# Optimization experiments

Hardware: AMD Instinct MI355X
Metric: run time of the kernel (lower is better)

The kernel has to match this reference:

```python
import jax, jax.numpy as jnp
import numpy as np

SCALE = 32.0
MARGIN = 0.25


def setup_inputs() -> dict:
    key = jax.random.key(0)
    k1, k2 = jax.random.split(key)
    feats = jax.random.normal(k1, (8192, 128), dtype=jnp.float32)
    labels = jax.random.randint(k2, (8192,), 0, 14, dtype=jnp.int64)
    return {"feats": feats, "labels": labels}


def reference(feats, labels):
    # cosine similarity: L2-normalize rows then GEMM  -> sim [B, B]
    f = feats / jnp.linalg.norm(feats, axis=1, keepdims=True)
    sim = f @ f.T

    B = feats.shape[0]
    same = labels[:, None] == labels[None, :]
    eye = jnp.eye(B, dtype=bool)
    pos_mask = same & ~eye          # same label, excluding self
    neg_mask = ~same                # different label

    s, m = SCALE, MARGIN
    alpha_p = jax.nn.relu(1.0 + m - sim)
    alpha_n = jax.nn.relu(sim + m)
    # exponents; masked-out entries set to -inf so exp -> 0 (matches masked sum)
    expo_p = jnp.where(pos_mask, -s * alpha_p * (sim - (1.0 - m)), -jnp.inf)
    expo_n = jnp.where(neg_mask, s * alpha_n * (sim - m), -jnp.inf)

    loss_p = jnp.sum(jnp.exp(expo_p), axis=1)   # [B]
    loss_n = jnp.sum(jnp.exp(expo_n), axis=1)   # [B]
    loss = jnp.mean(jnp.log1p(loss_p * loss_n))
    return loss
```

## Files before the change

kernel.cpp:

```cpp
#include <hip/hip_runtime.h>
#include <math.h>


#define DIM 128
typedef short bf16x8 __attribute__((ext_vector_type(8)));
typedef float f32x4 __attribute__((ext_vector_type(4)));

#if __has_builtin(__builtin_amdgcn_exp2f)
#define EXP2F __builtin_amdgcn_exp2f
#else
#define EXP2F exp2f
#endif

__device__ __forceinline__ unsigned short f2bf(float f) {
    unsigned int b = __float_as_uint(f);
    unsigned int r = (b + 0x7FFFu + ((b >> 16) & 1u)) >> 16;
    return (unsigned short)r;
}
__device__ __forceinline__ unsigned int packPN(float p, float n) {
    return (unsigned int)f2bf(p) | ((unsigned int)f2bf(n) << 16);
}

__global__ void prep_kernel(const float* __restrict__ feats,
                            unsigned int* __restrict__ featsN, int B) {
    int wave = (blockIdx.x * blockDim.x + threadIdx.x) >> 6;
    int lane = threadIdx.x & 63;
    if (wave >= B) return;
    const float2* rp = (const float2*)(feats + (size_t)wave * DIM);
    float2 v = rp[lane];
    float s = v.x * v.x + v.y * v.y;
#pragma unroll
    for (int off = 32; off; off >>= 1) s += __shfl_xor(s, off);
    float inv = rsqrtf(s);
    featsN[(size_t)wave * 64 + lane] =
        (unsigned int)f2bf(v.x * inv) | ((unsigned int)f2bf(v.y * inv) << 16);
}

__global__ __launch_bounds__(256, 3) void circle_main_kernel(
    const unsigned short* __restrict__ featsN, const int* __restrict__ labels,
    unsigned int* __restrict__ partial, int B) {
    __shared__ unsigned char smem[49152] __attribute__((aligned(16)));
    unsigned char* Al = smem;
    unsigned char* Bl = smem + 32768;
    unsigned int* tbuf = (unsigned int*)smem;

    int bid = blockIdx.x;
    int RT = (int)((129.0 - sqrt(16641.0 - 8.0 * (double)bid)) * 0.5);
    RT = RT < 0 ? 0 : (RT > 63 ? 63 : RT);
    while (64 * RT - (RT * (RT - 1)) / 2 > bid) --RT;
    while (64 * (RT + 1) - ((RT + 1) * RT) / 2 <= bid) ++RT;
    const int CT = RT + (bid - (64 * RT - (RT * (RT - 1)) / 2));
    const bool diag = (RT == CT);

    const int tid = threadIdx.x;
    const int lane = tid & 63;
    const int wv = tid >> 6;
    const int wr = wv >> 1, wc = wv & 1;
    const int lg = lane >> 4;
    const int l15 = lane & 15;
    const int rowbase = RT * 128 + wr * 64;

    {
        const int r0 = tid >> 4, cc = tid & 15;
#pragma unroll
        for (int it = 0; it < 8; ++it) {
            int row = it * 16 + r0;
            int swz = ((cc ^ r0) << 4);
            int4 va = *(const int4*)(featsN + (size_t)(RT * 128 + row) * DIM + cc * 8);
            *(int4*)(Al + row * 256 + swz) = va;
        }
    }

    int lr[4][4];
#pragma unroll
    for (int m = 0; m < 4; ++m)
#pragma unroll
        for (int r = 0; r < 4; ++r) lr[m][r] = labels[rowbase + m * 16 + lg * 4 + r];

    const float S2 = 46.166241308446828f;
    const float C2 = -23.083120654223414f;

    float rP[4][4], rN[4][4];
#pragma unroll
    for (int m = 0; m < 4; ++m)
#pragma unroll
        for (int r = 0; r < 4; ++r) { rP[m][r] = 0.f; rN[m][r] = 0.f; }

#pragma unroll
    for (int h = 0; h < 2; ++h) {
        __syncthreads();
        {
            const int r0 = tid >> 4, cc = tid & 15;
#pragma unroll
            for (int it = 0; it < 4; ++it) {
                int row = it * 16 + r0;
                int swz = ((cc ^ r0) << 4);
                int4 vb = *(const int4*)(featsN +
                    (size_t)(CT * 128 + h * 64 + row) * DIM + cc * 8);
                *(int4*)(Bl + row * 256 + swz) = vb;
            }
        }
        __syncthreads();

        f32x4 acc[4][2];
#pragma unroll
        for (int m = 0; m < 4; ++m)
#pragma unroll
            for (int n = 0; n < 2; ++n) acc[m][n] = (f32x4){0.f, 0.f, 0.f, 0.f};
#pragma unroll
        for (int kk = 0; kk < 4; ++kk) {
            bf16x8 af[4], bfr[2];
#pragma unroll
            for (int m = 0; m < 4; ++m) {
                int row = wr * 64 + m * 16 + l15;
                af[m] = __builtin_bit_cast(bf16x8,
                    *(const int4*)(Al + row * 256 + (((kk * 4 + lg) ^ l15) << 4)));
            }
#pragma unroll
            for (int n = 0; n < 2; ++n) {
                int row = wc * 32 + n * 16 + l15;
                bfr[n] = __builtin_bit_cast(bf16x8,
                    *(const int4*)(Bl + row * 256 + (((kk * 4 + lg) ^ l15) << 4)));
            }
#pragma unroll
            for (int m = 0; m < 4; ++m)
#pragma unroll
                for (int n = 0; n < 2; ++n)
                    acc[m][n] = __builtin_amdgcn_mfma_f32_16x16x32_bf16(
                        af[m], bfr[n], acc[m][n], 0, 0, 0);
        }

        const int colbase = CT * 128 + h * 64 + wc * 32;
        int lc[2];
#pragma unroll
        for (int n = 0; n < 2; ++n) lc[n] = labels[colbase + n * 16 + l15];

        if (diag) {
#pragma unroll
            for (int m = 0; m < 4; ++m) {
#pragma unroll
                for (int r = 0; r < 4; ++r) {
                    const int grow = rowbase + m * 16 + lg * 4 + r;
                    const int lrow = lr[m][r];
                    float psum = 0.f, nsum = 0.f;
#pragma unroll
                    for (int n = 0; n < 2; ++n) {
                        float sim = acc[m][n][r];
                        bool same = (lrow == lc[n]);
                        float u = same ? (1.25f - sim) : (sim + 0.25f);
                        float e2 = fmaxf(u, 0.f) * fmaf(S2, u, C2);
                        float v = EXP2F(e2);
                        bool self = (grow == colbase + n * 16 + l15);
                        float pv = (same && !self) ? v : 0.f;
                        float nv = same ? 0.f : v;
                        psum += pv; nsum += nv;
                    }
                    rP[m][r] += psum; rN[m][r] += nsum;
                }
            }
        } else {
            float cP[2] = {0.f, 0.f}, cN[2] = {0.f, 0.f};
#pragma unroll
            for (int m = 0; m < 4; ++m) {
#pragma unroll
                for (int r = 0; r < 4; ++r) {
                    const int lrow = lr[m][r];
                    float psum = 0.f, nsum = 0.f;
#pragma unroll
                    for (int n = 0; n < 2; ++n) {
                        float sim = acc[m][n][r];
                        bool same = (lrow == lc[n]);
                        float u = same ? (1.25f - sim) : (sim + 0.25f);
                        float e2 = fmaxf(u, 0.f) * fmaf(S2, u, C2);
                        float v = EXP2F(e2);
                        float pv = same ? v : 0.f;
                        float nv = v - pv;
                        psum += pv; nsum += nv;
                        cP[n] += pv; cN[n] += nv;
                    }
                    rP[m][r] += psum; rN[m][r] += nsum;
                }
            }
#pragma unroll
            for (int n = 0; n < 2; ++n) {
                float p = cP[n], n_ = cN[n];
                p += __shfl_xor(p, 16); p += __shfl_xor(p, 32);
                n_ += __shfl_xor(n_, 16); n_ += __shfl_xor(n_, 32);
                if (lg == 0) {
                    int gcol = colbase + n * 16 + l15;
                    partial[(size_t)(RT * 2 + wr) * B + gcol] = packPN(p, n_);
                }
            }
        }
    }

    __syncthreads();
    {
        unsigned int* T = tbuf + wv * 64 * 17;
#pragma unroll
        for (int m = 0; m < 4; ++m)
#pragma unroll
            for (int r = 0; r < 4; ++r)
                T[(m * 16 + lg * 4 + r) * 17 + l15] = packPN(rP[m][r], rN[m][r]);
    }
    __syncthreads();
    {
        const unsigned int* T = tbuf + wv * 64 * 17 + lane * 17;
        float p = 0.f, n_ = 0.f;
#pragma unroll
        for (int c = 0; c < 16; ++c) {
            unsigned int v = T[c];
            p += __uint_as_float(v << 16);
            n_ += __uint_as_float(v & 0xFFFF0000u);
        }
        int grow = RT * 128 + wr * 64 + lane;
        partial[(size_t)(CT * 2 + wc) * B + grow] = packPN(p, n_);
    }
}

__global__ void rowloss_kernel(const unsigned int* __restrict__ partial,
                               double* __restrict__ blocksum, int B) {
    int row = blockIdx.x * 64 + threadIdx.x;
    float p = 0.f, n = 0.f;
#pragma unroll
    for (int c = 0; c < 128; ++c) {
        unsigned int v = partial[(size_t)c * B + row];
        p += __uint_as_float(v << 16);
        n += __uint_as_float(v & 0xFFFF0000u);
    }
    double l = log1p((double)p * (double)n);
#pragma unroll
    for (int off = 32; off; off >>= 1) l += __shfl_xor(l, off);
    if (threadIdx.x == 0) blocksum[blockIdx.x] = l;
}

__global__ void final_kernel(const double* __restrict__ blocksum,
                             float* __restrict__ out, int nblk, int B) {
    __shared__ double sdata[128];
    int tid = threadIdx.x;
    sdata[tid] = (tid < nblk) ? blocksum[tid] : 0.0;
    __syncthreads();
    for (int s = 64; s; s >>= 1) {
        if (tid < s) sdata[tid] += sdata[tid + s];
        __syncthreads();
    }
    if (tid == 0) out[0] = (float)(sdata[0] / (double)B);
}

extern "C" void kernel_launch(void* const* d_in, const int* in_sizes, int n_in,
                              void* d_out, int out_size, void* d_ws, size_t ws_size,
                              hipStream_t stream) {
    const float* feats = (const float*)d_in[0];
    const int* labels = (const int*)d_in[1];
    float* out = (float*)d_out;
    int B = in_sizes[1];

    unsigned int* featsN = (unsigned int*)d_ws;
    size_t off1 = ((size_t)B * DIM * 2 + 255) & ~(size_t)255;
    unsigned int* partial = (unsigned int*)((char*)d_ws + off1);
    size_t off2 = off1 + (((size_t)B * 128 * sizeof(unsigned int) + 255) & ~(size_t)255);
    double* blocksum = (double*)((char*)d_ws + off2);

    prep_kernel<<<B / 4, 256, 0, stream>>>(feats, featsN, B);

    int ntiles = B / 128;
    int nblocks = ntiles * (ntiles + 1) / 2;
    circle_main_kernel<<<nblocks, 256, 0, stream>>>((const unsigned short*)featsN,
                                                    labels, partial, B);

    int nblk = B / 64;
    rowloss_kernel<<<nblk, 64, 0, stream>>>(partial, blocksum, B);
    final_kernel<<<1, 128, 0, stream>>>(blocksum, out, nblk, B);
}
```

Measured before the change: 44.27 us.

## Split triangular tiles into 128x64 blocks on a 2D grid with early exit

The main kernel now computes one 128x64 half-tile per block on a 2D grid instead of looping over two column halves of a 128x128 upper-triangular tile. Blocks below the diagonal return at once, and the triangular index decoding with sqrt is removed. The partial buffer grows to 384 slots so column partials get their own region, and the row-loss kernel reads only the slots that were written. This doubles the number of blocks for more parallelism and latency hiding, at the cost of reloading the A tile per half-tile, launching many empty blocks, and lowering the occupancy hint from 3 to 2.

```diff
diff --git a/kernel.cpp b/kernel.cpp
--- a/kernel.cpp
+++ b/kernel.cpp
@@ -3,6 +3,7 @@
 
 
 #define DIM 128
+#define NSLOT 384
 typedef short bf16x8 __attribute__((ext_vector_type(8)));
 typedef float f32x4 __attribute__((ext_vector_type(4)));
 
@@ -36,21 +37,18 @@
         (unsigned int)f2bf(v.x * inv) | ((unsigned int)f2bf(v.y * inv) << 16);
 }
 
-__global__ __launch_bounds__(256, 3) void circle_main_kernel(
+__global__ __launch_bounds__(256, 2) void circle_main_kernel(
     const unsigned short* __restrict__ featsN, const int* __restrict__ labels,
     unsigned int* __restrict__ partial, int B) {
+    const int C = blockIdx.x;
+    const int R = blockIdx.y;
+    if (C < 2 * R) return;
+    const bool diagType = ((C >> 1) == R);
+
     __shared__ unsigned char smem[49152] __attribute__((aligned(16)));
     unsigned char* Al = smem;
     unsigned char* Bl = smem + 32768;
     unsigned int* tbuf = (unsigned int*)smem;
-
-    int bid = blockIdx.x;
-    int RT = (int)((129.0 - sqrt(16641.0 - 8.0 * (double)bid)) * 0.5);
-    RT = RT < 0 ? 0 : (RT > 63 ? 63 : RT);
-    while (64 * RT - (RT * (RT - 1)) / 2 > bid) --RT;
-    while (64 * (RT + 1) - ((RT + 1) * RT) / 2 <= bid) ++RT;
-    const int CT = RT + (bid - (64 * RT - (RT * (RT - 1)) / 2));
-    const bool diag = (RT == CT);
 
     const int tid = threadIdx.x;
     const int lane = tid & 63;
@@ -58,17 +56,23 @@
     const int wr = wv >> 1, wc = wv & 1;
     const int lg = lane >> 4;
     const int l15 = lane & 15;
-    const int rowbase = RT * 128 + wr * 64;
+    const int rowbase = R * 128 + wr * 64;
 
     {
         const int r0 = tid >> 4, cc = tid & 15;
+        const int swz = ((cc ^ r0) << 4);
 #pragma unroll
         for (int it = 0; it < 8; ++it) {
             int row = it * 16 + r0;
-            int swz = ((cc ^ r0) << 4);
-            int4 va = *(const int4*)(featsN + (size_t)(RT * 128 + row) * DIM + cc * 8);
+            int4 va = *(const int4*)(featsN + (size_t)(R * 128 + row) * DIM + cc * 8);
             *(int4*)(Al + row * 256 + swz) = va;
         }
+#pragma unroll
+        for (int it = 0; it < 4; ++it) {
+            int row = it * 16 + r0;
+            int4 vb = *(const int4*)(featsN + (size_t)(C * 64 + row) * DIM + cc * 8);
+            *(int4*)(Bl + row * 256 + swz) = vb;
+        }
     }
 
     int lr[4][4];
@@ -77,119 +81,100 @@
 #pragma unroll
         for (int r = 0; r < 4; ++r) lr[m][r] = labels[rowbase + m * 16 + lg * 4 + r];
 
+    __syncthreads();
+
+    f32x4 acc[4][2];
+#pragma unroll
+    for (int m = 0; m < 4; ++m)
+#pragma unroll
+        for (int n = 0; n < 2; ++n) acc[m][n] = (f32x4){0.f, 0.f, 0.f, 0.f};
+#pragma unroll
+    for (int kk = 0; kk < 4; ++kk) {
+        bf16x8 af[4], bfr[2];
+#pragma unroll
+        for (int m = 0; m < 4; ++m) {
+            int row = wr * 64 + m * 16 + l15;
+            af[m] = __builtin_bit_cast(bf16x8,
+                *(const int4*)(Al + row * 256 + (((kk * 4 + lg) ^ l15) << 4)));
+        }
+#pragma unroll
+        for (int n = 0; n < 2; ++n) {
+            int row = wc * 32 + n * 16 + l15;
+            bfr[n] = __builtin_bit_cast(bf16x8,
+                *(const int4*)(Bl + row * 256 + (((kk * 4 + lg) ^ l15) << 4)));
+        }
+#pragma unroll
+        for (int m = 0; m < 4; ++m)
+#pragma unroll
+            for (int n = 0; n < 2; ++n)
+                acc[m][n] = __builtin_amdgcn_mfma_f32_16x16x32_bf16(
+                    af[m], bfr[n], acc[m][n], 0, 0, 0);
+    }
+
+    const int colbase = C * 64 + wc * 32;
     const float S2 = 46.166241308446828f;
     const float C2 = -23.083120654223414f;
 
+    int lc[2];
+#pragma unroll
+    for (int n = 0; n < 2; ++n) lc[n] = labels[colbase + n * 16 + l15];
+
     float rP[4][4], rN[4][4];
-#pragma unroll
-    for (int m = 0; m < 4; ++m)
-#pragma unroll
-        for (int r = 0; r < 4; ++r) { rP[m][r] = 0.f; rN[m][r] = 0.f; }
-
-#pragma unroll
-    for (int h = 0; h < 2; ++h) {
-        __syncthreads();
-        {
-            const int r0 = tid >> 4, cc = tid & 15;
-#pragma unroll
-            for (int it = 0; it < 4; ++it) {
-                int row = it * 16 + r0;
-                int swz = ((cc ^ r0) << 4);
-                int4 vb = *(const int4*)(featsN +
-                    (size_t)(CT * 128 + h * 64 + row) * DIM + cc * 8);
-                *(int4*)(Bl + row * 256 + swz) = vb;
+
+    if (diagType) {
+#pragma unroll
+        for (int m = 0; m < 4; ++m) {
+#pragma unroll
+            for (int r = 0; r < 4; ++r) {
+                const int grow = rowbase + m * 16 + lg * 4 + r;
+                const int lrow = lr[m][r];
+                float psum = 0.f, nsum = 0.f;
+#pragma unroll
+                for (int n = 0; n < 2; ++n) {
+                    float sim = acc[m][n][r];
+                    bool same = (lrow == lc[n]);
+                    float u = same ? (1.25f - sim) : (sim + 0.25f);
+                    float e2 = fmaxf(u, 0.f) * fmaf(S2, u, C2);
+                    float v = EXP2F(e2);
+                    bool self = (grow == colbase + n * 16 + l15);
+                    float pv = (same && !self) ? v : 0.f;
+                    float nv = same ? 0.f : v;
+                    psum += pv; nsum += nv;
+                }
+                rP[m][r] = psum; rN[m][r] = nsum;
             }
         }
-        __syncthreads();
-
-        f32x4 acc[4][2];
-#pragma unroll
-        for (int m = 0; m < 4; ++m)
-#pragma unroll
-            for (int n = 0; n < 2; ++n) acc[m][n] = (f32x4){0.f, 0.f, 0.f, 0.f};
-#pragma unroll
-        for (int kk = 0; kk < 4; ++kk) {
-            bf16x8 af[4], bfr[2];
-#pragma unroll
-            for (int m = 0; m < 4; ++m) {
-                int row = wr * 64 + m * 16 + l15;
-                af[m] = __builtin_bit_cast(bf16x8,
-                    *(const int4*)(Al + row * 256 + (((kk * 4 + lg) ^ l15) << 4)));
+    } else {
+        float cP[2] = {0.f, 0.f}, cN[2] = {0.f, 0.f};
+#pragma unroll
+        for (int m = 0; m < 4; ++m) {
+#pragma unroll
+            for (int r = 0; r < 4; ++r) {
+                const int lrow = lr[m][r];
+                float psum = 0.f, nsum = 0.f;
+#pragma unroll
+                for (int n = 0; n < 2; ++n) {
+                    float sim = acc[m][n][r];
+                    bool same = (lrow == lc[n]);
+                    float u = same ? (1.25f - sim) : (sim + 0.25f);
+                    float e2 = fmaxf(u, 0.f) * fmaf(S2, u, C2);
+                    float v = EXP2F(e2);
+                    float pv = same ? v : 0.f;
+                    float nv = v - pv;
+                    psum += pv; nsum += nv;
+                    cP[n] += pv; cN[n] += nv;
+                }
+                rP[m][r] = psum; rN[m][r] = nsum;
             }
-#pragma unroll
-            for (int n = 0; n < 2; ++n) {
-                int row = wc * 32 + n * 16 + l15;
-                bfr[n] = __builtin_bit_cast(bf16x8,
-                    *(const int4*)(Bl + row * 256 + (((kk * 4 + lg) ^ l15) << 4)));
-            }
-#pragma unroll
-            for (int m = 0; m < 4; ++m)
-#pragma unroll
-                for (int n = 0; n < 2; ++n)
-                    acc[m][n] = __builtin_amdgcn_mfma_f32_16x16x32_bf16(
-                        af[m], bfr[n], acc[m][n], 0, 0, 0);
-        }
-
-        const int colbase = CT * 128 + h * 64 + wc * 32;
-        int lc[2];
-#pragma unroll
-        for (int n = 0; n < 2; ++n) lc[n] = labels[colbase + n * 16 + l15];
-
-        if (diag) {
-#pragma unroll
-            for (int m = 0; m < 4; ++m) {
-#pragma unroll
-                for (int r = 0; r < 4; ++r) {
-                    const int grow = rowbase + m * 16 + lg * 4 + r;
-                    const int lrow = lr[m][r];
-                    float psum = 0.f, nsum = 0.f;
-#pragma unroll
-                    for (int n = 0; n < 2; ++n) {
-                        float sim = acc[m][n][r];
-                        bool same = (lrow == lc[n]);
-                        float u = same ? (1.25f - sim) : (sim + 0.25f);
-                        float e2 = fmaxf(u, 0.f) * fmaf(S2, u, C2);
-                        float v = EXP2F(e2);
-                        bool self = (grow == colbase + n * 16 + l15);
-                        float pv = (same && !self) ? v : 0.f;
-                        float nv = same ? 0.f : v;
-                        psum += pv; nsum += nv;
-                    }
-                    rP[m][r] += psum; rN[m][r] += nsum;
-                }
-            }
-        } else {
-            float cP[2] = {0.f, 0.f}, cN[2] = {0.f, 0.f};
-#pragma unroll
-            for (int m = 0; m < 4; ++m) {
-#pragma unroll
-                for (int r = 0; r < 4; ++r) {
-                    const int lrow = lr[m][r];
-                    float psum = 0.f, nsum = 0.f;
-#pragma unroll
-                    for (int n = 0; n < 2; ++n) {
-                        float sim = acc[m][n][r];
-                        bool same = (lrow == lc[n]);
-                        float u = same ? (1.25f - sim) : (sim + 0.25f);
-                        float e2 = fmaxf(u, 0.f) * fmaf(S2, u, C2);
-                        float v = EXP2F(e2);
-                        float pv = same ? v : 0.f;
-                        float nv = v - pv;
-                        psum += pv; nsum += nv;
-                        cP[n] += pv; cN[n] += nv;
-                    }
-                    rP[m][r] += psum; rN[m][r] += nsum;
-                }
-            }
-#pragma unroll
-            for (int n = 0; n < 2; ++n) {
-                float p = cP[n], n_ = cN[n];
-                p += __shfl_xor(p, 16); p += __shfl_xor(p, 32);
-                n_ += __shfl_xor(n_, 16); n_ += __shfl_xor(n_, 32);
-                if (lg == 0) {
-                    int gcol = colbase + n * 16 + l15;
-                    partial[(size_t)(RT * 2 + wr) * B + gcol] = packPN(p, n_);
-                }
+        }
+#pragma unroll
+        for (int n = 0; n < 2; ++n) {
+            float p = cP[n], n_ = cN[n];
+            p += __shfl_xor(p, 16); p += __shfl_xor(p, 32);
+            n_ += __shfl_xor(n_, 16); n_ += __shfl_xor(n_, 32);
+            if (lg == 0) {
+                int gcol = colbase + n * 16 + l15;
+                partial[(size_t)(256 + R * 2 + wr) * B + gcol] = packPN(p, n_);
             }
         }
     }
@@ -213,17 +198,24 @@
             p += __uint_as_float(v << 16);
             n_ += __uint_as_float(v & 0xFFFF0000u);
         }
-        int grow = RT * 128 + wr * 64 + lane;
-        partial[(size_t)(CT * 2 + wc) * B + grow] = packPN(p, n_);
+        int grow = R * 128 + wr * 64 + lane;
+        partial[(size_t)(C * 2 + wc) * B + grow] = packPN(p, n_);
     }
 }
 
 __global__ void rowloss_kernel(const unsigned int* __restrict__ partial,
                                double* __restrict__ blocksum, int B) {
     int row = blockIdx.x * 64 + threadIdx.x;
+    int RTg = row >> 7;
+    int Cg = row >> 6;
     float p = 0.f, n = 0.f;
-#pragma unroll
-    for (int c = 0; c < 128; ++c) {
+    for (int c = 4 * RTg; c < 256; ++c) {
+        unsigned int v = partial[(size_t)c * B + row];
+        p += __uint_as_float(v << 16);
+        n += __uint_as_float(v & 0xFFFF0000u);
+    }
+    int kmax = (Cg >= 2) ? ((((Cg - 2) >> 1) + 1) << 1) : 0;
+    for (int c = 256; c < 256 + kmax; ++c) {
         unsigned int v = partial[(size_t)c * B + row];
         p += __uint_as_float(v << 16);
         n += __uint_as_float(v & 0xFFFF0000u);
@@ -258,15 +250,14 @@
     unsigned int* featsN = (unsigned int*)d_ws;
     size_t off1 = ((size_t)B * DIM * 2 + 255) & ~(size_t)255;
     unsigned int* partial = (unsigned int*)((char*)d_ws + off1);
-    size_t off2 = off1 + (((size_t)B * 128 * sizeof(unsigned int) + 255) & ~(size_t)255);
+    size_t off2 = off1 + (((size_t)B * NSLOT * sizeof(unsigned int) + 255) & ~(size_t)255);
     double* blocksum = (double*)((char*)d_ws + off2);
 
     prep_kernel<<<B / 4, 256, 0, stream>>>(feats, featsN, B);
 
-    int ntiles = B / 128;
-    int nblocks = ntiles * (ntiles + 1) / 2;
-    circle_main_kernel<<<nblocks, 256, 0, stream>>>((const unsigned short*)featsN,
-                                                    labels, partial, B);
+    dim3 grid(128, 64);
+    circle_main_kernel<<<grid, 256, 0, stream>>>((const unsigned short*)featsN,
+                                                 labels, partial, B);
 
     int nblk = B / 64;
     rowloss_kernel<<<nblk, 64, 0, stream>>>(partial, blocksum, B);
```

New measurement: 101.7 us. +129.7%, slower.
